# Performance work log

Measured on AMD Instinct MI355X. Metric: run time of the kernel, lower is better.

Reference implementation:

```python
import jax, jax.numpy as jnp
import numpy as np

IN_FT = 256
OUT_FT = 256


def setup_inputs() -> dict:
    key = jax.random.key(0)
    k1, k2, k3 = jax.random.split(key, 3)
    B, N = 4, 4096
    seq = jax.random.normal(k1, (B, N, IN_FT), dtype=jnp.float32)
    adj = jax.random.uniform(k2, (B, N, N), dtype=jnp.float32)
    # Xavier-uniform fc weight [out_ft, in_ft], bias zeros
    limit = float(np.sqrt(6.0 / (IN_FT + OUT_FT)))
    W = jax.random.uniform(k3, (OUT_FT, IN_FT), minval=-limit, maxval=limit, dtype=jnp.float32)
    b = jnp.zeros((OUT_FT,), dtype=jnp.float32)
    alpha = jnp.array(0.25, dtype=jnp.float32)  # PReLU shared parameter
    return {"seq": seq, "adj": adj, "W": W, "b": b, "alpha": alpha}


def reference(seq, adj, W, b, alpha):
    # Linear projection: [B, N, out_ft]
    h = jnp.einsum("bni,oi->bno", seq, W) + b
    # Neighbor aggregation (dense bmm path): [B, N, N] @ [B, N, out_ft]
    h = jnp.einsum("bnm,bmo->bno", adj, h)
    # PReLU with shared alpha
    return jnp.where(h > 0, h, alpha * h)
```

## Files before the change

### kernel.cpp

```cpp
#include <hip/hip_runtime.h>
#include <hip/hip_bf16.h>

#define NSEQ 4096
#define FT 256
#define BKB 128

typedef __attribute__((ext_vector_type(8))) short bf16x8;
typedef __attribute__((ext_vector_type(4))) float f32x4;

__device__ __forceinline__ ushort f2bf(float f) {
  __hip_bfloat16 h = __float2bfloat16(f);
  return *reinterpret_cast<const ushort*>(&h);
}

__device__ __forceinline__ int swz(int row, int byteInRow) {
  return row * 128 + (byteInRow ^ ((row & 7) << 4));
}

__global__ __launch_bounds__(512) void transpose_cast_kernel(
    const float* __restrict__ seq, ushort* __restrict__ seqT) {
  __shared__ __align__(16) ushort lT[256 * 72];

  const int tid = threadIdx.x;
  const int batch = blockIdx.x >> 6;
  const int n0 = (blockIdx.x & 63) * 64;
  const float* src = seq + ((size_t)batch * NSEQ + n0) * FT;

  const int ar = tid >> 3, ac = tid & 7;
#pragma unroll
  for (int p = 0; p < 8; ++p) {
    const int fb = (ac + p * 8) * 4;
    f32x4 v = *reinterpret_cast<const f32x4*>(src + (size_t)ar * FT + fb);
#pragma unroll
    for (int e = 0; e < 4; ++e) lT[(fb + e) * 72 + ar] = f2bf(v[e]);
  }
  __syncthreads();
  const int f = tid >> 1, hf = tid & 1;
  ushort* dst = seqT + ((size_t)(batch * FT + f)) * NSEQ + n0 + hf * 32;
#pragma unroll
  for (int k = 0; k < 4; ++k) {
    uint4 v = *reinterpret_cast<const uint4*>(&lT[f * 72 + hf * 32 + k * 8]);
    *reinterpret_cast<uint4*>(dst + k * 8) = v;
  }
}

__global__ __launch_bounds__(512) void bmm_prelu_kernel(
    const float* __restrict__ adj, const ushort* __restrict__ seqT,
    const float* __restrict__ W, const float* __restrict__ bias,
    const float* __restrict__ alphaP, float* __restrict__ out) {
  __shared__ __align__(16) char smem[2 * 65536 + 2 * 16384];

  const int tid = threadIdx.x;
  const int lane = tid & 63;
  const int wid = tid >> 6;
  const int wm = wid >> 2, wn = wid & 3;

  const int bid = blockIdx.x;
  const int sbid = (bid & 7) * 32 + (bid >> 3);
  const int batch = sbid >> 6;
  const int m0 = (sbid & 63) * 64;

  const float* adjB = adj + (size_t)batch * NSEQ * NSEQ + (size_t)m0 * NSEQ;
  const ushort* hTB = seqT + (size_t)batch * FT * NSEQ;

  auto lB = [&](int i) -> char* { return smem + i * 65536; };
  auto lA = [&](int i) -> char* { return smem + 131072 + i * 16384; };

  const int arow = tid >> 3, ac = tid & 7;
  const int bro = (lane >> 4);
  const int bhalf = (lane >> 3) & 1;
  f32x4 rS[4];
  float rsum = 0.f;

  f32x4 acc[2][4];
  const f32x4 zero = {0.f, 0.f, 0.f, 0.f};
#pragma unroll
  for (int mi = 0; mi < 2; ++mi)
#pragma unroll
    for (int ni = 0; ni < 4; ++ni) acc[mi][ni] = zero;

  auto issueA = [&](int t) {
    const int k0 = t * BKB;
#pragma unroll
    for (int q = 0; q < 4; ++q)
      rS[q] = *reinterpret_cast<const f32x4*>(
          adjB + (size_t)arow * NSEQ + k0 + ac * 16 + q * 4);
  };
  auto issueB = [&](int t, int ib) {
    const int k0 = t * BKB;
#pragma unroll
    for (int p = 0; p < 8; ++p) {
      const int grow = wid * 32 + p * 4 + bro;
      const int gsrc = (lane & 7) ^ (((p & 1) * 4 + bro) & 7);
      const ushort* gp = hTB + (size_t)grow * NSEQ + k0 + bhalf * 64 + gsrc * 8;
      char* lp = lB(ib) + wid * 8192 + p * 1024;
      __builtin_amdgcn_global_load_lds(
          (const __attribute__((address_space(1))) void*)gp,
          (__attribute__((address_space(3))) void*)lp, 16, 0, 0);
    }
  };
  auto writeA = [&](int ia) {
    char* lAp = lA(ia);
    const int half = ac >> 2;
#pragma unroll
    for (int q = 0; q < 4; ++q) {
      rsum += rS[q][0] + rS[q][1] + rS[q][2] + rS[q][3];
      ushort4 u = make_ushort4(f2bf(rS[q][0]), f2bf(rS[q][1]),
                               f2bf(rS[q][2]), f2bf(rS[q][3]));
      const int gih = (((ac & 3) * 2 + (q >> 1)) ^ (arow & 7));
      *reinterpret_cast<ushort4*>(lAp + arow * 256 + half * 128 + gih * 16 +
                                  (q & 1) * 8) = u;
    }
  };
  auto mma32 = [&](const char* lAp, const char* lBp) {
    const int r16 = lane & 15;
    const int sub = lane >> 4;
#pragma unroll
    for (int kk = 0; kk < 4; ++kk) {
      const int half = kk >> 1;
      const int gih = (((kk & 1) * 4 + sub) ^ (r16 & 7));
      const int bofs = half * 128 + gih * 16;
      bf16x8 a[2], b[4];
#pragma unroll
      for (int mi = 0; mi < 2; ++mi) {
        const int row = wm * 32 + mi * 16 + r16;
        a[mi] = *reinterpret_cast<const bf16x8*>(lAp + row * 256 + bofs);
      }
#pragma unroll
      for (int ni = 0; ni < 4; ++ni) {
        const int row = wn * 64 + ni * 16 + r16;
        b[ni] = *reinterpret_cast<const bf16x8*>(lBp + row * 256 + bofs);
      }
#pragma unroll
      for (int mi = 0; mi < 2; ++mi)
#pragma unroll
        for (int ni = 0; ni < 4; ++ni)
          acc[mi][ni] = __builtin_amdgcn_mfma_f32_16x16x32_bf16(
              a[mi], b[ni], acc[mi][ni], 0, 0, 0);
    }
  };

  issueA(0);
  __builtin_amdgcn_sched_barrier(0);
  issueB(0, 0);
  __builtin_amdgcn_sched_barrier(0);
  asm volatile("s_waitcnt vmcnt(8)" ::: "memory");
  __builtin_amdgcn_sched_barrier(0);
  writeA(0);
  asm volatile("s_waitcnt vmcnt(0) lgkmcnt(0)" ::: "memory");
  __builtin_amdgcn_s_barrier();
  __builtin_amdgcn_sched_barrier(0);

  auto body = [&](int t, int cur) {
    issueA(t + 1);
    __builtin_amdgcn_sched_barrier(0);
    issueB(t + 1, cur ^ 1);
    __builtin_amdgcn_sched_barrier(0);
    __builtin_amdgcn_s_setprio(1);
    mma32(lA(cur), lB(cur));
    __builtin_amdgcn_s_setprio(0);
    asm volatile("s_waitcnt vmcnt(8)" ::: "memory");
    __builtin_amdgcn_sched_barrier(0);
    writeA(cur ^ 1);
    asm volatile("s_waitcnt vmcnt(0) lgkmcnt(0)" ::: "memory");
    __builtin_amdgcn_s_barrier();
    __builtin_amdgcn_sched_barrier(0);
  };

  for (int j = 0; j < 15; ++j) {
    body(2 * j, 0);
    body(2 * j + 1, 1);
  }
  body(30, 0);
  __builtin_amdgcn_s_setprio(1);
  mma32(lA(1), lB(1));
  __builtin_amdgcn_s_setprio(0);

  const float alpha = *alphaP;
  __syncthreads();

  ushort* lT64 = (ushort*)smem;
  float* rsP = (float*)(smem + 98304);
  float* rsW = (float*)(smem + 100352);
  const int TP2 = 264;
#pragma unroll
  for (int mi = 0; mi < 2; ++mi) {
    const int rbase = wm * 32 + mi * 16 + ((lane >> 4) << 2);
#pragma unroll
    for (int ni = 0; ni < 4; ++ni) {
      const int f = wn * 64 + ni * 16 + (lane & 15);
#pragma unroll
      for (int j = 0; j < 4; ++j) lT64[(rbase + j) * TP2 + f] = f2bf(acc[mi][ni][j]);
    }
  }
  rsP[arow * 8 + ac] = rsum;
  __syncthreads();
  if (tid < 64) {
    float s = 0.f;
#pragma unroll
    for (int i = 0; i < 8; ++i) s += rsP[tid * 8 + i];
    rsW[tid] = s;
  }

  ushort* lW = (ushort*)(smem + 49152);
  f32x4 accO[2][4];
#pragma unroll
  for (int mi = 0; mi < 2; ++mi)
#pragma unroll
    for (int ni = 0; ni < 4; ++ni) accO[mi][ni] = zero;
  const int war = tid >> 4, wac = tid & 15;
  for (int c = 0; c < 4; ++c) {
    __syncthreads();
    f32x4 rW[8];
#pragma unroll
    for (int p = 0; p < 8; ++p)
      rW[p] = *reinterpret_cast<const f32x4*>(
          W + (size_t)(war + p * 32) * FT + c * 64 + wac * 4);
#pragma unroll
    for (int p = 0; p < 8; ++p) {
      ushort4 u = make_ushort4(f2bf(rW[p][0]), f2bf(rW[p][1]),
                               f2bf(rW[p][2]), f2bf(rW[p][3]));
      *reinterpret_cast<ushort4*>((char*)lW + swz(war + p * 32, wac * 8)) = u;
    }
    __syncthreads();
    const int r16 = lane & 15;
    const int g16 = (lane >> 4) * 16;
#pragma unroll
    for (int kk = 0; kk < 2; ++kk) {
      const int kb = kk * 64 + g16;
      const int fo = c * 64 + kk * 32 + (lane >> 4) * 8;
      bf16x8 a[2], b[4];
#pragma unroll
      for (int mi = 0; mi < 2; ++mi) {
        const int row = wm * 32 + mi * 16 + r16;
        a[mi] = *reinterpret_cast<const bf16x8*>(&lT64[row * TP2 + fo]);
      }
#pragma unroll
      for (int ni = 0; ni < 4; ++ni) {
        const int row = wn * 64 + ni * 16 + r16;
        b[ni] = *reinterpret_cast<const bf16x8*>((char*)lW + swz(row, kb));
      }
#pragma unroll
      for (int mi = 0; mi < 2; ++mi)
#pragma unroll
        for (int ni = 0; ni < 4; ++ni)
          accO[mi][ni] = __builtin_amdgcn_mfma_f32_16x16x32_bf16(
              a[mi], b[ni], accO[mi][ni], 0, 0, 0);
    }
  }

  __syncthreads();
  float* lo = (float*)smem;
  const int PITCH = 264;
#pragma unroll
  for (int mi = 0; mi < 2; ++mi) {
    const int rbase = wm * 32 + mi * 16 + ((lane >> 4) << 2);
#pragma unroll
    for (int ni = 0; ni < 4; ++ni) {
      const int o = wn * 64 + ni * 16 + (lane & 15);
      const float bo = bias[o];
#pragma unroll
      for (int j = 0; j < 4; ++j) {
        float v = accO[mi][ni][j] + bo * rsW[rbase + j];
        v = v > 0.f ? v : alpha * v;
        lo[(rbase + j) * PITCH + o] = v;
      }
    }
  }
  __syncthreads();
  float* outB = out + ((size_t)batch * NSEQ + m0) * FT;
  const int r = tid >> 3, c8 = tid & 7;
#pragma unroll
  for (int k = 0; k < 8; ++k) {
    const int g = c8 + k * 8;
    f32x4 v = *reinterpret_cast<const f32x4*>(lo + r * PITCH + g * 4);
    __builtin_nontemporal_store(v, reinterpret_cast<f32x4*>(outB + (size_t)r * FT + g * 4));
  }
}

extern "C" void kernel_launch(void* const* d_in, const int* in_sizes, int n_in,
                              void* d_out, int out_size, void* d_ws, size_t ws_size,
                              hipStream_t stream) {
  const float* seq = (const float*)d_in[0];
  const float* adj = (const float*)d_in[1];
  const float* W = (const float*)d_in[2];
  const float* bias = (const float*)d_in[3];
  const float* alpha = (const float*)d_in[4];
  float* out = (float*)d_out;
  ushort* seqT = (ushort*)d_ws;

  transpose_cast_kernel<<<256, 512, 0, stream>>>(seq, seqT);
  bmm_prelu_kernel<<<256, 512, 0, stream>>>(adj, seqT, W, bias, alpha, out);
}
```

Baseline: 83.34 us.

## Prefetch adj tiles two iterations ahead using double register buffers

Splits the adj register staging into two register sets so each fp32 adj tile load is issued two k-steps ahead instead of one. The vmcnt waits are reordered so B's LDS loads are issued first, and the epilogue iteration is peeled. The goal is to hide global-memory latency of the large fp32 adjacency stream behind more MFMA work. It costs 16 more VGPRs per thread, which could lower occupancy or cause spills.

Measured after the change: 84.80 us. About the same (+1.7%).

```diff
diff --git a/kernel.cpp b/kernel.cpp
--- a/kernel.cpp
+++ b/kernel.cpp
@@ -69,7 +69,7 @@
   const int arow = tid >> 3, ac = tid & 7;
   const int bro = (lane >> 4);
   const int bhalf = (lane >> 3) & 1;
-  f32x4 rS[4];
+  f32x4 rS0[4], rS1[4];
   float rsum = 0.f;
 
   f32x4 acc[2][4];
@@ -79,11 +79,11 @@
 #pragma unroll
     for (int ni = 0; ni < 4; ++ni) acc[mi][ni] = zero;
 
-  auto issueA = [&](int t) {
+  auto issueA = [&](int t, f32x4* r) {
     const int k0 = t * BKB;
 #pragma unroll
     for (int q = 0; q < 4; ++q)
-      rS[q] = *reinterpret_cast<const f32x4*>(
+      r[q] = *reinterpret_cast<const f32x4*>(
           adjB + (size_t)arow * NSEQ + k0 + ac * 16 + q * 4);
   };
   auto issueB = [&](int t, int ib) {
@@ -99,14 +99,14 @@
           (__attribute__((address_space(3))) void*)lp, 16, 0, 0);
     }
   };
-  auto writeA = [&](int ia) {
+  auto writeA = [&](const f32x4* r, int ia) {
     char* lAp = lA(ia);
     const int half = ac >> 2;
 #pragma unroll
     for (int q = 0; q < 4; ++q) {
-      rsum += rS[q][0] + rS[q][1] + rS[q][2] + rS[q][3];
-      ushort4 u = make_ushort4(f2bf(rS[q][0]), f2bf(rS[q][1]),
-                               f2bf(rS[q][2]), f2bf(rS[q][3]));
+      rsum += r[q][0] + r[q][1] + r[q][2] + r[q][3];
+      ushort4 u = make_ushort4(f2bf(r[q][0]), f2bf(r[q][1]),
+                               f2bf(r[q][2]), f2bf(r[q][3]));
       const int gih = (((ac & 3) * 2 + (q >> 1)) ^ (arow & 7));
       *reinterpret_cast<ushort4*>(lAp + arow * 256 + half * 128 + gih * 16 +
                                   (q & 1) * 8) = u;
@@ -140,38 +140,53 @@
     }
   };
 
-  issueA(0);
-  __builtin_amdgcn_sched_barrier(0);
   issueB(0, 0);
   __builtin_amdgcn_sched_barrier(0);
-  asm volatile("s_waitcnt vmcnt(8)" ::: "memory");
-  __builtin_amdgcn_sched_barrier(0);
-  writeA(0);
-  asm volatile("s_waitcnt vmcnt(0) lgkmcnt(0)" ::: "memory");
+  issueA(0, rS0);
+  __builtin_amdgcn_sched_barrier(0);
+  issueA(1, rS1);
+  __builtin_amdgcn_sched_barrier(0);
+  asm volatile("s_waitcnt vmcnt(4)" ::: "memory");
+  __builtin_amdgcn_sched_barrier(0);
+  writeA(rS0, 0);
+  asm volatile("s_waitcnt lgkmcnt(0)" ::: "memory");
   __builtin_amdgcn_s_barrier();
   __builtin_amdgcn_sched_barrier(0);
 
-  auto body = [&](int t, int cur) {
-    issueA(t + 1);
-    __builtin_amdgcn_sched_barrier(0);
+  auto body = [&](int t, int cur, f32x4* rIss, const f32x4* rWr) {
     issueB(t + 1, cur ^ 1);
+    __builtin_amdgcn_sched_barrier(0);
+    issueA(t + 2, rIss);
     __builtin_amdgcn_sched_barrier(0);
     __builtin_amdgcn_s_setprio(1);
     mma32(lA(cur), lB(cur));
     __builtin_amdgcn_s_setprio(0);
+    asm volatile("s_waitcnt vmcnt(12)" ::: "memory");
+    __builtin_amdgcn_sched_barrier(0);
+    writeA(rWr, cur ^ 1);
+    asm volatile("s_waitcnt vmcnt(4)" ::: "memory");
+    asm volatile("s_waitcnt lgkmcnt(0)" ::: "memory");
+    __builtin_amdgcn_s_barrier();
+    __builtin_amdgcn_sched_barrier(0);
+  };
+
+  for (int j = 0; j < 15; ++j) {
+    body(2 * j, 0, rS0, rS1);
+    body(2 * j + 1, 1, rS1, rS0);
+  }
+  {
+    issueB(31, 1);
+    __builtin_amdgcn_sched_barrier(0);
+    __builtin_amdgcn_s_setprio(1);
+    mma32(lA(0), lB(0));
+    __builtin_amdgcn_s_setprio(0);
     asm volatile("s_waitcnt vmcnt(8)" ::: "memory");
     __builtin_amdgcn_sched_barrier(0);
-    writeA(cur ^ 1);
+    writeA(rS1, 1);
     asm volatile("s_waitcnt vmcnt(0) lgkmcnt(0)" ::: "memory");
     __builtin_amdgcn_s_barrier();
     __builtin_amdgcn_sched_barrier(0);
-  };
-
-  for (int j = 0; j < 15; ++j) {
-    body(2 * j, 0);
-    body(2 * j + 1, 1);
-  }
-  body(30, 0);
+  }
   __builtin_amdgcn_s_setprio(1);
   mma32(lA(1), lB(1));
   __builtin_amdgcn_s_setprio(0);
```
